# Kernel optimization log

Measured on AMD Instinct MI355X. Metric: run time of the kernel, lower is better.

## Reference

```python
import jax, jax.numpy as jnp
import numpy as np

D_MODEL = 1024
D_STATE = 16
D_CONV = 4
EXPAND = 2
D_INNER = D_MODEL * EXPAND


def setup_inputs() -> dict:
    key = jax.random.key(0)
    ks = jax.random.split(key, 8)
    B, L = 2, 2048
    x = jax.random.normal(ks[0], (B, L, D_MODEL), dtype=jnp.float32)
    # in_proj: Linear(d_model -> 2*d_inner), no bias
    W_in = jax.random.normal(ks[1], (D_MODEL, 2 * D_INNER), dtype=jnp.float32) / np.sqrt(D_MODEL)
    # depthwise conv1d: (d_inner, 1, d_conv) + bias
    conv_w = jax.random.normal(ks[2], (D_INNER, 1, D_CONV), dtype=jnp.float32) / np.sqrt(D_CONV)
    conv_b = jax.random.normal(ks[3], (D_INNER,), dtype=jnp.float32) * 0.01
    # x_proj: Linear(d_inner -> 2*d_state + 1), no bias
    W_x = jax.random.normal(ks[4], (D_INNER, 2 * D_STATE + 1), dtype=jnp.float32) / np.sqrt(D_INNER)
    # A_log ~ Uniform(-log(d_state), -1)
    A_log = jax.random.uniform(ks[5], (D_INNER, D_STATE), dtype=jnp.float32,
                               minval=-np.log(D_STATE), maxval=-1.0)
    D_param = jnp.ones((D_INNER,), dtype=jnp.float32)
    W_out = jax.random.normal(ks[6], (D_INNER, D_MODEL), dtype=jnp.float32) / np.sqrt(D_INNER)
    return {"x": x, "W_in": W_in, "conv_w": conv_w, "conv_b": conv_b,
            "W_x": W_x, "A_log": A_log, "D_param": D_param, "W_out": W_out}


def _selective_scan(x, delta, A, Bm, Cm):
    # x:(B,L,D), delta:(B,L), A:(D,N), Bm/Cm:(B,L,N)
    Bsz, L, Dd = x.shape
    N = A.shape[1]
    h0 = jnp.zeros((Bsz, Dd, N), dtype=x.dtype)

    def step(h, inp):
        dt, Bt, Ct, xt = inp  # (B,), wait dt:(B,), Bt:(B,N), Ct:(B,N), xt:(B,D)
        A_bar = jnp.exp(dt[:, None, None] * A)          # (B,D,N)
        dB = (dt[:, None] * Bt)[:, None, :]             # (B,1,N)
        h = A_bar * h + dB * xt[:, :, None]             # (B,D,N)
        y = jnp.einsum('bn,bdn->bd', Ct, h)             # (B,D)
        return h, y

    xs = (jnp.swapaxes(delta, 0, 1), jnp.swapaxes(Bm, 0, 1),
          jnp.swapaxes(Cm, 0, 1), jnp.swapaxes(x, 0, 1))
    _, ys = jax.lax.scan(step, h0, xs)                  # ys: (L,B,D)
    return jnp.swapaxes(ys, 0, 1)


def reference(x, W_in, conv_w, conv_b, W_x, A_log, D_param, W_out):
    B, L, _ = x.shape
    xr = x @ W_in                                       # (B,L,2*Di)
    x_inner, res = jnp.split(xr, 2, axis=-1)
    # causal depthwise conv: left-pad d_conv-1, valid conv == torch slice [:L]
    xc = jnp.swapaxes(x_inner, 1, 2)                    # (B,Di,L)
    xc = jax.lax.conv_general_dilated(
        xc, conv_w, window_strides=(1,), padding=[(D_CONV - 1, 0)],
        dimension_numbers=('NCH', 'OIH', 'NCH'), feature_group_count=D_INNER)
    xc = xc + conv_b[None, :, None]
    xc = jnp.swapaxes(xc, 1, 2)                         # (B,L,Di)
    xc = jax.nn.silu(xc)
    ssm_params = xc @ W_x                               # (B,L,1+2N)
    delta = jax.nn.softplus(ssm_params[..., 0])         # (B,L)
    Bm = ssm_params[..., 1:1 + D_STATE]                 # (B,L,N)
    Cm = ssm_params[..., 1 + D_STATE:]                  # (B,L,N)
    A = -jnp.exp(A_log)                                 # (Di,N)
    y = _selective_scan(xc, delta, A, Bm, Cm)           # (B,L,Di)
    y = y + xc * D_param[None, None, :]
    y = y * jax.nn.silu(res)
    return y @ W_out                                    # (B,L,d_model)
```

## Files before the change

### kernel.cpp

```cpp
#include <hip/hip_runtime.h>

#define L_SEQ 2048
#define NB    2
#define DMOD  1024
#define DIN   2048
#define NST   16
#define NROWS (NB*L_SEQ)
#define CL    64
#define NC    (L_SEQ/CL)

typedef unsigned short u16;
typedef _Float16 half8 __attribute__((ext_vector_type(8)));
typedef float f32x4 __attribute__((ext_vector_type(4)));
typedef short short8 __attribute__((ext_vector_type(8)));

__device__ __forceinline__ float siluf(float v){ return v / (1.f + __expf(-v)); }
__device__ __forceinline__ u16 f2h_bits(float v){ _Float16 h = (_Float16)v; return __builtin_bit_cast(u16, h); }
__device__ __forceinline__ float h2f(u16 v){ return (float)__builtin_bit_cast(_Float16, v); }
__device__ __forceinline__ float fexp2(float x){
#if __has_builtin(__builtin_amdgcn_exp2f)
    return __builtin_amdgcn_exp2f(x);
#else
    return __expf(x * 0.69314718056f);
#endif
}

__device__ __forceinline__ void gload16(const u16* g, u16* l)
{
    __builtin_amdgcn_global_load_lds(
        (const __attribute__((address_space(1))) void*)g,
        (__attribute__((address_space(3))) void*)l,
        16, 0, 0);
}

__global__ __launch_bounds__(256)
void f32_to_f16(const float* __restrict__ in, u16* __restrict__ out, int n4)
{
    int i = blockIdx.x * 256 + threadIdx.x;
    if (i >= n4) return;
    float4 v = ((const float4*)in)[i];
    ushort4 o;
    o.x = f2h_bits(v.x); o.y = f2h_bits(v.y); o.z = f2h_bits(v.z); o.w = f2h_bits(v.w);
    *(ushort4*)&out[(size_t)i * 4] = o;
}

__global__ __launch_bounds__(256)
void transpose_to_f16(const float* __restrict__ in, u16* __restrict__ outT, int R, int C)
{
    __shared__ float s[64][65];
    int r0 = blockIdx.y * 64, c0 = blockIdx.x * 64;
    int tc = threadIdx.x & 63, ty = threadIdx.x >> 6;
    #pragma unroll
    for (int j = 0; j < 16; j++) {
        int r = ty + j * 4;
        s[r][tc] = in[(size_t)(r0 + r) * C + c0 + tc];
    }
    __syncthreads();
    #pragma unroll
    for (int j = 0; j < 16; j++) {
        int nn = ty + j * 4;
        outT[(size_t)(c0 + nn) * R + r0 + tc] = f2h_bits(s[tc][nn]);
    }
}

template<int BN, int EPI>
__global__ __launch_bounds__(256)
void gemm_mfma(const u16* __restrict__ A, const u16* __restrict__ Bt,
               void* __restrict__ C0v, void* __restrict__ C1v,
               int M, int N, int K)
{
    constexpr int NI = BN / 32;
    __shared__ __align__(16) u16 As0[128 * 64], As1[128 * 64];
    __shared__ __align__(16) u16 Bs0[BN * 64],  Bs1[BN * 64];
    const int tid  = threadIdx.x;
    const int lane = tid & 63;
    const int wid  = tid >> 6;
    const int wm   = wid >> 1, wn = wid & 1;
    const int bm = blockIdx.y * 128, bn = blockIdx.x * BN;

    const int srow8 = lane >> 3;
    const int sunit = (lane & 7) ^ srow8;
    const u16* Ag = A  + (size_t)(bm + srow8) * K + sunit * 8;
    const u16* Bg = Bt + (size_t)(bn + srow8) * K + sunit * 8;

    const int fr = lane & 15;
    const int s0 = (((lane >> 4) ^ (lane & 7))) * 8;
    const int aBase = (wm * 64 + fr) * 64 + s0;
    const int bBase = (wn * (BN / 2) + fr) * 64 + s0;

    f32x4 acc[4][NI];
    #pragma unroll
    for (int i = 0; i < 4; i++)
        #pragma unroll
        for (int j = 0; j < NI; j++)
            acc[i][j] = (f32x4){0.f, 0.f, 0.f, 0.f};

    auto STAGE = [&](u16* Ab, u16* Bb, int k0) {
        #pragma unroll
        for (int j = 0; j < 4; j++) {
            int c = wid * 4 + j;
            gload16(Ag + (size_t)(c * 8) * K + k0, Ab + c * 512);
        }
        #pragma unroll
        for (int j = 0; j < NI; j++) {
            int c = wid * NI + j;
            gload16(Bg + (size_t)(c * 8) * K + k0, Bb + c * 512);
        }
    };

    auto COMPUTE = [&](const u16* Ab, const u16* Bb) {
        #pragma unroll
        for (int kk = 0; kk < 2; kk++) {
            const int x = kk ? 32 : 0;
            half8 af[4], bf[NI];
            #pragma unroll
            for (int mi = 0; mi < 4; mi++)
                af[mi] = *(const half8*)&Ab[(aBase ^ x) + mi * 1024];
            #pragma unroll
            for (int ni = 0; ni < NI; ni++)
                bf[ni] = *(const half8*)&Bb[(bBase ^ x) + ni * 1024];
            #pragma unroll
            for (int mi = 0; mi < 4; mi++)
                #pragma unroll
                for (int ni = 0; ni < NI; ni++)
                    acc[mi][ni] = __builtin_amdgcn_mfma_f32_16x16x32_f16(af[mi], bf[ni], acc[mi][ni], 0, 0, 0);
        }
    };

    const int NT = K >> 6;
    STAGE(As0, Bs0, 0);
    __syncthreads();
    for (int t = 0; t < NT; t += 2) {
        if (t + 1 < NT) STAGE(As1, Bs1, (t + 1) << 6);
        COMPUTE(As0, Bs0);
        __syncthreads();
        if (t + 2 < NT) STAGE(As0, Bs0, (t + 2) << 6);
        if (t + 1 < NT) COMPUTE(As1, Bs1);
        __syncthreads();
    }

    const int cr = (lane >> 4) * 4;
    const int cc = lane & 15;
    #pragma unroll
    for (int mi = 0; mi < 4; mi++) {
        #pragma unroll
        for (int ni = 0; ni < NI; ni++) {
            #pragma unroll
            for (int q = 0; q < 4; q++) {
                int row = bm + wm * 64 + mi * 16 + cr + q;
                int col = bn + wn * (BN / 2) + ni * 16 + cc;
                float v = acc[mi][ni][q];
                if (EPI == 0) {
                    ((float*)C0v)[(size_t)row * N + col] = v;
                } else {
                    int half = N >> 1;
                    if (col < half) ((u16*)C0v)[(size_t)row * half + col] = f2h_bits(v);
                    else            ((u16*)C1v)[(size_t)row * half + col - half] = f2h_bits(siluf(v));
                }
            }
        }
    }
}

__global__ __launch_bounds__(256)
void conv_silu16(const u16* __restrict__ xin16, const float* __restrict__ cw,
                 const float* __restrict__ cb, u16* __restrict__ xc16)
{
    int idx = blockIdx.x * 256 + threadIdx.x;
    int d8 = idx & 255;
    int t  = (idx >> 8) & (L_SEQ - 1);
    int b  = idx >> 19;
    int d  = d8 << 3;
    const float4* cw4 = (const float4*)cw;
    float4 w[8];
    #pragma unroll
    for (int j = 0; j < 8; j++) w[j] = cw4[d + j];
    float acc[8];
    {
        float4 b0 = *(const float4*)&cb[d];
        float4 b1 = *(const float4*)&cb[d + 4];
        acc[0]=b0.x; acc[1]=b0.y; acc[2]=b0.z; acc[3]=b0.w;
        acc[4]=b1.x; acc[5]=b1.y; acc[6]=b1.z; acc[7]=b1.w;
    }
    #pragma unroll
    for (int k = 0; k < 4; k++) {
        int tt = t + k - 3;
        if (tt >= 0) {
            short8 v = *(const short8*)&xin16[((size_t)(b * L_SEQ + tt)) * DIN + d];
            #pragma unroll
            for (int j = 0; j < 8; j++)
                acc[j] = fmaf(h2f((u16)v[j]), (&w[j].x)[k], acc[j]);
        }
    }
    short8 o;
    #pragma unroll
    for (int j = 0; j < 8; j++) o[j] = (short)f2h_bits(siluf(acc[j]));
    *(short8*)&xc16[(size_t)idx * 8] = o;
}

__global__ __launch_bounds__(256)
void transpose_wx16(const float* __restrict__ Wx, u16* __restrict__ WxT16)
{
    int idx = blockIdx.x * 256 + threadIdx.x;
    int n = idx >> 11, k = idx & 2047;
    float v = (n < 33) ? Wx[k * 33 + n] : 0.f;
    WxT16[idx] = f2h_bits(v);
}

__global__ __launch_bounds__(256)
void gemm2_mfma(const u16* __restrict__ A, const u16* __restrict__ Bt, float* __restrict__ pb)
{
    __shared__ __align__(16) u16 As[64 * 64];
    __shared__ __align__(16) u16 Bs[48 * 64];
    const int tid = threadIdx.x, lane = tid & 63, w = tid >> 6;
    const int bm = blockIdx.x * 64;
    const int kz = blockIdx.y;
    const int arow = tid >> 2;
    const int au   = (tid & 3) << 1;
    f32x4 acc[3];
    acc[0] = acc[1] = acc[2] = (f32x4){0.f, 0.f, 0.f, 0.f};

    for (int it = 0; it < 4; ++it) {
        const int k0 = kz * 256 + it * 64;
        short8 ra0 = *(const short8*)&A[(size_t)(bm + arow) * DIN + k0 + au * 8];
        short8 ra1 = *(const short8*)&A[(size_t)(bm + arow) * DIN + k0 + (au + 1) * 8];
        short8 rb0, rb1;
        if (tid < 192) {
            rb0 = *(const short8*)&Bt[(size_t)arow * DIN + k0 + au * 8];
            rb1 = *(const short8*)&Bt[(size_t)arow * DIN + k0 + (au + 1) * 8];
        }
        __syncthreads();
        {
            int s0 = au ^ (arow & 7), s1 = (au + 1) ^ (arow & 7);
            *(short8*)&As[arow * 64 + s0 * 8] = ra0;
            *(short8*)&As[arow * 64 + s1 * 8] = ra1;
            if (tid < 192) {
                *(short8*)&Bs[arow * 64 + s0 * 8] = rb0;
                *(short8*)&Bs[arow * 64 + s1 * 8] = rb1;
            }
        }
        __syncthreads();
        #pragma unroll
        for (int kk = 0; kk < 2; kk++) {
            int r = w * 16 + (lane & 15);
            int sl = (kk * 4 + (lane >> 4)) ^ (r & 7);
            half8 af = *(const half8*)&As[r * 64 + sl * 8];
            #pragma unroll
            for (int ni = 0; ni < 3; ni++) {
                int br = ni * 16 + (lane & 15);
                int bsl = (kk * 4 + (lane >> 4)) ^ (br & 7);
                half8 bf = *(const half8*)&Bs[br * 64 + bsl * 8];
                acc[ni] = __builtin_amdgcn_mfma_f32_16x16x32_f16(af, bf, acc[ni], 0, 0, 0);
            }
        }
    }
    #pragma unroll
    for (int ni = 0; ni < 3; ni++) {
        #pragma unroll
        for (int q = 0; q < 4; q++) {
            int row = bm + w * 16 + (lane >> 4) * 4 + q;
            int col = ni * 16 + (lane & 15);
            pb[((size_t)kz * NROWS + row) * 48 + col] = acc[ni][q];
        }
    }
}

__global__ __launch_bounds__(256)
void gemm2_reduce(const float* __restrict__ pb, float* __restrict__ delta,
                  float* __restrict__ Bm, float* __restrict__ Cm)
{
    int idx = blockIdx.x * 256 + threadIdx.x;
    int row = idx / 48, col = idx - row * 48;
    float s = 0.f;
    #pragma unroll
    for (int kz = 0; kz < 8; kz++) s += pb[(size_t)kz * NROWS * 48 + idx];
    if (col == 0)       delta[row] = fmaxf(s, 0.f) + log1pf(__expf(-fabsf(s)));
    else if (col < 17)  Bm[row * NST + col - 1]  = s;
    else if (col < 33)  Cm[row * NST + col - 17] = s;
}

__global__ __launch_bounds__(256)
void scan_part1_reg(const u16* __restrict__ xc16, const float* __restrict__ delta,
                    const float* __restrict__ Bm, const float* __restrict__ A_log,
                    float* __restrict__ h_loc, float* __restrict__ Pc)
{
    const int b = blockIdx.z, c = blockIdx.y;
    const int d = blockIdx.x * 256 + threadIdx.x;
    float ka[16];
    {
        const float4* Av = (const float4*)(A_log + (size_t)d * 16);
        #pragma unroll
        for (int q = 0; q < 4; q++) {
            float4 a = Av[q];
            ka[q*4+0] = -__expf(a.x) * 1.44269504f;
            ka[q*4+1] = -__expf(a.y) * 1.44269504f;
            ka[q*4+2] = -__expf(a.z) * 1.44269504f;
            ka[q*4+3] = -__expf(a.w) * 1.44269504f;
        }
    }
    float h[16];
    #pragma unroll
    for (int n = 0; n < 16; n++) h[n] = 0.f;
    float S = 0.f;
    const int rowbase = b * L_SEQ + c * CL;
    #pragma unroll 2
    for (int t = 0; t < CL; ++t) {
        const int rowg = rowbase + t;
        const float dt = delta[rowg];
        const float4* Bv = (const float4*)(Bm + (size_t)rowg * 16);
        float4 b0 = Bv[0], b1 = Bv[1], b2 = Bv[2], b3 = Bv[3];
        float bb[16] = {b0.x,b0.y,b0.z,b0.w, b1.x,b1.y,b1.z,b1.w,
                        b2.x,b2.y,b2.z,b2.w, b3.x,b3.y,b3.z,b3.w};
        const float xt = h2f(xc16[(size_t)rowg * DIN + d]);
        const float dtx = dt * xt;
        S += dt;
        #pragma unroll
        for (int n = 0; n < 16; n++) {
            float a = fexp2(dt * ka[n]);
            h[n] = fmaf(a, h[n], bb[n] * dtx);
        }
    }
    float* hp = h_loc + (((size_t)(b * NC + c) * DIN) + d) * 16;
    float* pp = Pc    + (((size_t)(b * NC + c) * DIN) + d) * 16;
    #pragma unroll
    for (int q = 0; q < 4; q++) {
        *(float4*)&hp[q*4] = (float4){h[q*4+0], h[q*4+1], h[q*4+2], h[q*4+3]};
        *(float4*)&pp[q*4] = (float4){fexp2(S*ka[q*4+0]), fexp2(S*ka[q*4+1]),
                                      fexp2(S*ka[q*4+2]), fexp2(S*ka[q*4+3])};
    }
}

__global__ __launch_bounds__(256)
void scan_carry(const float* __restrict__ h_loc, const float* __restrict__ Pc,
                float* __restrict__ H_in)
{
    int gid = blockIdx.x * 256 + threadIdx.x;
    int b = gid >> 15, r = gid & 32767;
    float H = 0.f;
    for (int c = 0; c < NC; ++c) {
        size_t idx = ((size_t)(b * NC + c) << 15) + r;
        H_in[idx] = H;
        H = fmaf(Pc[idx], H, h_loc[idx]);
    }
}

__global__ __launch_bounds__(256)
void scan_part3_reg(const u16* __restrict__ xc16, const float* __restrict__ delta,
                    const float* __restrict__ Bm, const float* __restrict__ Cm,
                    const float* __restrict__ A_log, const float* __restrict__ Dp,
                    const u16* __restrict__ res16, const float* __restrict__ H_in,
                    u16* __restrict__ yh)
{
    const int b = blockIdx.z, c = blockIdx.y;
    const int d = blockIdx.x * 256 + threadIdx.x;
    float ka[16];
    {
        const float4* Av = (const float4*)(A_log + (size_t)d * 16);
        #pragma unroll
        for (int q = 0; q < 4; q++) {
            float4 a = Av[q];
            ka[q*4+0] = -__expf(a.x) * 1.44269504f;
            ka[q*4+1] = -__expf(a.y) * 1.44269504f;
            ka[q*4+2] = -__expf(a.z) * 1.44269504f;
            ka[q*4+3] = -__expf(a.w) * 1.44269504f;
        }
    }
    float h[16];
    {
        const float4* Hv = (const float4*)(H_in + (((size_t)(b * NC + c) * DIN) + d) * 16);
        #pragma unroll
        for (int q = 0; q < 4; q++) {
            float4 v = Hv[q];
            h[q*4+0]=v.x; h[q*4+1]=v.y; h[q*4+2]=v.z; h[q*4+3]=v.w;
        }
    }
    const float Dpd = Dp[d];
    const int rowbase = b * L_SEQ + c * CL;
    #pragma unroll 2
    for (int t = 0; t < CL; ++t) {
        const int rowg = rowbase + t;
        const float dt = delta[rowg];
        const float4* Bv = (const float4*)(Bm + (size_t)rowg * 16);
        const float4* Cv = (const float4*)(Cm + (size_t)rowg * 16);
        float4 b0 = Bv[0], b1 = Bv[1], b2 = Bv[2], b3 = Bv[3];
        float4 c0 = Cv[0], c1 = Cv[1], c2 = Cv[2], c3 = Cv[3];
        float bb[16] = {b0.x,b0.y,b0.z,b0.w, b1.x,b1.y,b1.z,b1.w,
                        b2.x,b2.y,b2.z,b2.w, b3.x,b3.y,b3.z,b3.w};
        float cc[16] = {c0.x,c0.y,c0.z,c0.w, c1.x,c1.y,c1.z,c1.w,
                        c2.x,c2.y,c2.z,c2.w, c3.x,c3.y,c3.z,c3.w};
        const float xt = h2f(xc16[(size_t)rowg * DIN + d]);
        const float rt = h2f(res16[(size_t)rowg * DIN + d]);
        const float dtx = dt * xt;
        float y = 0.f;
        #pragma unroll
        for (int n = 0; n < 16; n++) {
            float a = fexp2(dt * ka[n]);
            h[n] = fmaf(a, h[n], bb[n] * dtx);
            y = fmaf(cc[n], h[n], y);
        }
        y = (y + xt * Dpd) * rt;
        yh[(size_t)rowg * DIN + d] = f2h_bits(y);
    }
}

extern "C" void kernel_launch(void* const* d_in, const int* in_sizes, int n_in,
                              void* d_out, int out_size, void* d_ws, size_t ws_size,
                              hipStream_t stream)
{
    const float* x     = (const float*)d_in[0];
    const float* W_in  = (const float*)d_in[1];
    const float* cw    = (const float*)d_in[2];
    const float* cb    = (const float*)d_in[3];
    const float* Wx    = (const float*)d_in[4];
    const float* A_log = (const float*)d_in[5];
    const float* Dp    = (const float*)d_in[6];
    const float* W_out = (const float*)d_in[7];
    float* out = (float*)d_out;
    float* ws  = (float*)d_ws;

    u16*   xin16 = (u16*)(ws);
    u16*   y16   = (u16*)(ws);
    u16*   res16 = (u16*)(ws + 4194304);
    u16*   xc16  = (u16*)(ws + 8388608);
    u16*   x16   = (u16*)(ws + 12582912);
    u16*   Bt3   = (u16*)(ws + 12582912);
    u16*   Bt1   = (u16*)(ws + 14680064);
    float* pb    = ws + 14680064;
    u16*   WxT16 = (u16*)(ws + 16777216);
    float* delta = ws + 16826368;
    float* Bm    = ws + 16830464;
    float* Cm    = ws + 16896000;
    float* h_loc = ws + 16961536;
    float* Pc    = ws + 19058688;
    float* H_in  = ws + 21155840;

    dim3 blk(256);

    f32_to_f16<<<dim3(NROWS * DMOD / 4 / 256), blk, 0, stream>>>(x, x16, NROWS * DMOD / 4);
    transpose_to_f16<<<dim3(4096 / 64, 1024 / 64), blk, 0, stream>>>(W_in, Bt1, DMOD, 2 * DIN);
    gemm_mfma<128, 1><<<dim3(32, 32), blk, 0, stream>>>(x16, Bt1, xin16, res16, NROWS, 2 * DIN, DMOD);
    conv_silu16<<<dim3(NB * L_SEQ * (DIN / 8) / 256), blk, 0, stream>>>(xin16, cw, cb, xc16);
    transpose_wx16<<<dim3(48 * DIN / 256), blk, 0, stream>>>(Wx, WxT16);
    gemm2_mfma<<<dim3(NROWS / 64, 8), blk, 0, stream>>>(xc16, WxT16, pb);
    gemm2_reduce<<<dim3(NROWS * 48 / 256), blk, 0, stream>>>(pb, delta, Bm, Cm);
    scan_part1_reg<<<dim3(DIN / 256, NC, NB), blk, 0, stream>>>(xc16, delta, Bm, A_log, h_loc, Pc);
    scan_carry<<<dim3(NB * DIN * NST / 256), blk, 0, stream>>>(h_loc, Pc, H_in);
    scan_part3_reg<<<dim3(DIN / 256, NC, NB), blk, 0, stream>>>(xc16, delta, Bm, Cm, A_log, Dp, res16, H_in, y16);
    transpose_to_f16<<<dim3(1024 / 64, 2048 / 64), blk, 0, stream>>>(W_out, Bt3, DIN, DMOD);
    gemm_mfma<64, 0><<<dim3(1024 / 64, NROWS / 128), blk, 0, stream>>>(y16, Bt3, out, nullptr, NROWS, DMOD, DIN);
}
```

Measured before the change: 210.9 us.

## Merge input prep kernels and split-K the output projection GEMM

Folds the x conversion, the W_in/W_out transposes and the W_x transpose into a single prep_inputs launch, cutting three kernel launches. The final GEMM switches from a 64-wide N tile to a 128-wide tile with a split-K of two, writing fp16 partials. A new add_partials kernel sums the partials into fp32. This trades launch overhead and a grid that was limited to 512 blocks for extra partial traffic, one more launch, and fp16 rounding of the partial sums.

Measured after the change: 213.2 us. About the same (+1.1%).

```diff
diff --git a/kernel.cpp b/kernel.cpp
--- a/kernel.cpp
+++ b/kernel.cpp
@@ -34,32 +34,41 @@
 }
 
 __global__ __launch_bounds__(256)
-void f32_to_f16(const float* __restrict__ in, u16* __restrict__ out, int n4)
-{
-    int i = blockIdx.x * 256 + threadIdx.x;
-    if (i >= n4) return;
-    float4 v = ((const float4*)in)[i];
-    ushort4 o;
-    o.x = f2h_bits(v.x); o.y = f2h_bits(v.y); o.z = f2h_bits(v.z); o.w = f2h_bits(v.w);
-    *(ushort4*)&out[(size_t)i * 4] = o;
-}
-
-__global__ __launch_bounds__(256)
-void transpose_to_f16(const float* __restrict__ in, u16* __restrict__ outT, int R, int C)
+void prep_inputs(const float* __restrict__ x, const float* __restrict__ W_in,
+                 const float* __restrict__ W_out, const float* __restrict__ Wx,
+                 u16* __restrict__ x16, u16* __restrict__ Bt1,
+                 u16* __restrict__ Bt3, u16* __restrict__ WxT16)
 {
     __shared__ float s[64][65];
-    int r0 = blockIdx.y * 64, c0 = blockIdx.x * 64;
-    int tc = threadIdx.x & 63, ty = threadIdx.x >> 6;
-    #pragma unroll
-    for (int j = 0; j < 16; j++) {
-        int r = ty + j * 4;
-        s[r][tc] = in[(size_t)(r0 + r) * C + c0 + tc];
-    }
-    __syncthreads();
-    #pragma unroll
-    for (int j = 0; j < 16; j++) {
-        int nn = ty + j * 4;
-        outT[(size_t)(c0 + nn) * R + r0 + tc] = f2h_bits(s[tc][nn]);
+    const int bid = blockIdx.x, tid = threadIdx.x;
+    if (bid < 4096) {
+        int i = bid * 256 + tid;
+        float4 v = ((const float4*)x)[i];
+        ushort4 o;
+        o.x = f2h_bits(v.x); o.y = f2h_bits(v.y); o.z = f2h_bits(v.z); o.w = f2h_bits(v.w);
+        *(ushort4*)&x16[(size_t)i * 4] = o;
+    } else if (bid < 5632) {
+        const float* in; u16* outT; int R, C, rblk, cblk;
+        if (bid < 5120) { int b = bid - 4096; in = W_in;  outT = Bt1; R = 1024; C = 4096; cblk = b & 63; rblk = b >> 6; }
+        else            { int b = bid - 5120; in = W_out; outT = Bt3; R = 2048; C = 1024; cblk = b & 15; rblk = b >> 4; }
+        int r0 = rblk * 64, c0 = cblk * 64;
+        int tc = tid & 63, ty = tid >> 6;
+        #pragma unroll
+        for (int j = 0; j < 16; j++) {
+            int r = ty + j * 4;
+            s[r][tc] = in[(size_t)(r0 + r) * C + c0 + tc];
+        }
+        __syncthreads();
+        #pragma unroll
+        for (int j = 0; j < 16; j++) {
+            int nn = ty + j * 4;
+            outT[(size_t)(c0 + nn) * R + r0 + tc] = f2h_bits(s[tc][nn]);
+        }
+    } else {
+        int idx = (bid - 5632) * 256 + tid;
+        int n = idx >> 11, k = idx & 2047;
+        float v = (n < 33) ? Wx[k * 33 + n] : 0.f;
+        WxT16[idx] = f2h_bits(v);
     }
 }
 
@@ -67,7 +76,7 @@
 __global__ __launch_bounds__(256)
 void gemm_mfma(const u16* __restrict__ A, const u16* __restrict__ Bt,
                void* __restrict__ C0v, void* __restrict__ C1v,
-               int M, int N, int K)
+               int M, int N, int KLEN, int lda, int ldb)
 {
     constexpr int NI = BN / 32;
     __shared__ __align__(16) u16 As0[128 * 64], As1[128 * 64];
@@ -77,11 +86,12 @@
     const int wid  = tid >> 6;
     const int wm   = wid >> 1, wn = wid & 1;
     const int bm = blockIdx.y * 128, bn = blockIdx.x * BN;
+    const int kBase = blockIdx.z * KLEN;
 
     const int srow8 = lane >> 3;
     const int sunit = (lane & 7) ^ srow8;
-    const u16* Ag = A  + (size_t)(bm + srow8) * K + sunit * 8;
-    const u16* Bg = Bt + (size_t)(bn + srow8) * K + sunit * 8;
+    const u16* Ag = A  + (size_t)(bm + srow8) * lda + kBase + sunit * 8;
+    const u16* Bg = Bt + (size_t)(bn + srow8) * ldb + kBase + sunit * 8;
 
     const int fr = lane & 15;
     const int s0 = (((lane >> 4) ^ (lane & 7))) * 8;
@@ -99,12 +109,12 @@
         #pragma unroll
         for (int j = 0; j < 4; j++) {
             int c = wid * 4 + j;
-            gload16(Ag + (size_t)(c * 8) * K + k0, Ab + c * 512);
+            gload16(Ag + (size_t)(c * 8) * lda + k0, Ab + c * 512);
         }
         #pragma unroll
         for (int j = 0; j < NI; j++) {
             int c = wid * NI + j;
-            gload16(Bg + (size_t)(c * 8) * K + k0, Bb + c * 512);
+            gload16(Bg + (size_t)(c * 8) * ldb + k0, Bb + c * 512);
         }
     };
 
@@ -127,7 +137,7 @@
         }
     };
 
-    const int NT = K >> 6;
+    const int NT = KLEN >> 6;
     STAGE(As0, Bs0, 0);
     __syncthreads();
     for (int t = 0; t < NT; t += 2) {
@@ -150,16 +160,35 @@
                 int row = bm + wm * 64 + mi * 16 + cr + q;
                 int col = bn + wn * (BN / 2) + ni * 16 + cc;
                 float v = acc[mi][ni][q];
-                if (EPI == 0) {
-                    ((float*)C0v)[(size_t)row * N + col] = v;
-                } else {
+                if (EPI == 1) {
                     int half = N >> 1;
                     if (col < half) ((u16*)C0v)[(size_t)row * half + col] = f2h_bits(v);
                     else            ((u16*)C1v)[(size_t)row * half + col - half] = f2h_bits(siluf(v));
+                } else {
+                    ((u16*)C0v)[((size_t)blockIdx.z * M + row) * N + col] = f2h_bits(v);
                 }
             }
         }
     }
+}
+
+__global__ __launch_bounds__(256)
+void add_partials(const u16* __restrict__ p, float* __restrict__ out)
+{
+    int i = blockIdx.x * 256 + threadIdx.x;
+    short8 a = *(const short8*)&p[(size_t)i * 8];
+    short8 b = *(const short8*)&p[(size_t)NROWS * DMOD + (size_t)i * 8];
+    float4 o0, o1;
+    o0.x = h2f((u16)a[0]) + h2f((u16)b[0]);
+    o0.y = h2f((u16)a[1]) + h2f((u16)b[1]);
+    o0.z = h2f((u16)a[2]) + h2f((u16)b[2]);
+    o0.w = h2f((u16)a[3]) + h2f((u16)b[3]);
+    o1.x = h2f((u16)a[4]) + h2f((u16)b[4]);
+    o1.y = h2f((u16)a[5]) + h2f((u16)b[5]);
+    o1.z = h2f((u16)a[6]) + h2f((u16)b[6]);
+    o1.w = h2f((u16)a[7]) + h2f((u16)b[7]);
+    *(float4*)&out[(size_t)i * 8]     = o0;
+    *(float4*)&out[(size_t)i * 8 + 4] = o1;
 }
 
 __global__ __launch_bounds__(256)
@@ -196,15 +225,6 @@
     #pragma unroll
     for (int j = 0; j < 8; j++) o[j] = (short)f2h_bits(siluf(acc[j]));
     *(short8*)&xc16[(size_t)idx * 8] = o;
-}
-
-__global__ __launch_bounds__(256)
-void transpose_wx16(const float* __restrict__ Wx, u16* __restrict__ WxT16)
-{
-    int idx = blockIdx.x * 256 + threadIdx.x;
-    int n = idx >> 11, k = idx & 2047;
-    float v = (n < 33) ? Wx[k * 33 + n] : 0.f;
-    WxT16[idx] = f2h_bits(v);
 }
 
 __global__ __launch_bounds__(256)
@@ -423,7 +443,7 @@
     u16*   res16 = (u16*)(ws + 4194304);
     u16*   xc16  = (u16*)(ws + 8388608);
     u16*   x16   = (u16*)(ws + 12582912);
-    u16*   Bt3   = (u16*)(ws + 12582912);
+    u16*   p     = (u16*)(ws + 12582912);
     u16*   Bt1   = (u16*)(ws + 14680064);
     float* pb    = ws + 14680064;
     u16*   WxT16 = (u16*)(ws + 16777216);
@@ -433,19 +453,20 @@
     float* h_loc = ws + 16961536;
     float* Pc    = ws + 19058688;
     float* H_in  = ws + 21155840;
+    u16*   Bt3   = (u16*)(ws + 23252992);
 
     dim3 blk(256);
 
-    f32_to_f16<<<dim3(NROWS * DMOD / 4 / 256), blk, 0, stream>>>(x, x16, NROWS * DMOD / 4);
-    transpose_to_f16<<<dim3(4096 / 64, 1024 / 64), blk, 0, stream>>>(W_in, Bt1, DMOD, 2 * DIN);
-    gemm_mfma<128, 1><<<dim3(32, 32), blk, 0, stream>>>(x16, Bt1, xin16, res16, NROWS, 2 * DIN, DMOD);
+    prep_inputs<<<dim3(6016), blk, 0, stream>>>(x, W_in, W_out, Wx, x16, Bt1, Bt3, WxT16);
+    gemm_mfma<128, 1><<<dim3(32, 32), blk, 0, stream>>>(x16, Bt1, xin16, res16,
+                                                        NROWS, 2 * DIN, DMOD, DMOD, DMOD);
     conv_silu16<<<dim3(NB * L_SEQ * (DIN / 8) / 256), blk, 0, stream>>>(xin16, cw, cb, xc16);
-    transpose_wx16<<<dim3(48 * DIN / 256), blk, 0, stream>>>(Wx, WxT16);
     gemm2_mfma<<<dim3(NROWS / 64, 8), blk, 0, stream>>>(xc16, WxT16, pb);
     gemm2_reduce<<<dim3(NROWS * 48 / 256), blk, 0, stream>>>(pb, delta, Bm, Cm);
     scan_part1_reg<<<dim3(DIN / 256, NC, NB), blk, 0, stream>>>(xc16, delta, Bm, A_log, h_loc, Pc);
     scan_carry<<<dim3(NB * DIN * NST / 256), blk, 0, stream>>>(h_loc, Pc, H_in);
     scan_part3_reg<<<dim3(DIN / 256, NC, NB), blk, 0, stream>>>(xc16, delta, Bm, Cm, A_log, Dp, res16, H_in, y16);
-    transpose_to_f16<<<dim3(1024 / 64, 2048 / 64), blk, 0, stream>>>(W_out, Bt3, DIN, DMOD);
-    gemm_mfma<64, 0><<<dim3(1024 / 64, NROWS / 128), blk, 0, stream>>>(y16, Bt3, out, nullptr, NROWS, DMOD, DIN);
-}
+    gemm_mfma<128, 2><<<dim3(DMOD / 128, NROWS / 128, 2), blk, 0, stream>>>(y16, Bt3, p, nullptr,
+                                                                            NROWS, DMOD, DIN / 2, DIN, DIN);
+    add_partials<<<dim3(NROWS * DMOD / 8 / 256), blk, 0, stream>>>(p, out);
+}
```
